# Kernel tuning notes

Hardware: AMD Instinct MI355X
Metric: run time of the kernel (lower is better)

The kernel has to match this reference:

```python
import jax, jax.numpy as jnp
import numpy as np

B, S, E = 4, 2048, 1024

def setup_inputs() -> dict:
    key = jax.random.key(0)
    ks = jax.random.split(key, 7)
    sc = 1.0 / np.sqrt(E)
    return {
        "x": jax.random.normal(ks[0], (B, S, E), dtype=jnp.float32),
        "wq_w": jax.random.normal(ks[1], (E, E), dtype=jnp.float32) * sc,
        "wq_b": jax.random.normal(ks[2], (E,), dtype=jnp.float32) * 0.01,
        "wk_w": jax.random.normal(ks[3], (E, E), dtype=jnp.float32) * sc,
        "wk_b": jax.random.normal(ks[4], (E,), dtype=jnp.float32) * 0.01,
        "wv_w": jax.random.normal(ks[5], (E, E), dtype=jnp.float32) * sc,
        "wv_b": jax.random.normal(ks[6], (E,), dtype=jnp.float32) * 0.01,
    }

def reference(x, wq_w, wq_b, wk_w, wk_b, wv_w, wv_b):
    # Linear projections (torch nn.Linear: y = x @ W^T + b)
    Q = jnp.einsum('bse,fe->bsf', x, wq_w) + wq_b
    K = jnp.einsum('bse,fe->bsf', x, wk_w) + wk_b
    V = jnp.einsum('bse,fe->bsf', x, wv_w) + wv_b
    # scaled dot-product attention, full [B, S, S] scores (single head)
    scores = jnp.einsum('bqe,bke->bqk', Q, K) / jnp.sqrt(jnp.asarray(Q.shape[-1], Q.dtype))
    attn = jax.nn.softmax(scores, axis=-1)
    return jnp.einsum('bqk,bke->bqe', attn, V)
```

## Files before the change

### kernel.cpp

```cpp
#include <hip/hip_runtime.h>
#include <hip/hip_bf16.h>
#include <stdint.h>

#define B_ 4
#define S_ 2048
#define E_ 1024


typedef __bf16 bf16;
typedef __attribute__((ext_vector_type(8))) __bf16 bf16x8;
typedef __attribute__((ext_vector_type(4))) float f32x4;
typedef __attribute__((ext_vector_type(4))) float float4v;
typedef __attribute__((ext_vector_type(4))) unsigned int uint4v;
typedef __attribute__((ext_vector_type(4))) unsigned short ushort4v;

__device__ inline unsigned short f2bf(float f) {
  union { float f; unsigned int u; } c; c.f = f;
  unsigned int u = c.u;
  unsigned int r = (u + 0x7FFFu + ((u >> 16) & 1u)) >> 16;
  return (unsigned short)r;
}

__device__ inline void load16_to_lds(const void* g, void* l) {
  __builtin_amdgcn_global_load_lds(
      (const __attribute__((address_space(1))) void*)g,
      (__attribute__((address_space(3))) void*)l,
      16, 0, 0);
}

__global__ __launch_bounds__(256) void cvt_all(
    const float* __restrict__ x, const float* __restrict__ w0,
    const float* __restrict__ w1, const float* __restrict__ w2,
    unsigned short* __restrict__ out, float* __restrict__ rowsum) {
  if (blockIdx.x >= 11264) {
    rowsum[(blockIdx.x - 11264) * 256 + threadIdx.x] = 0.f;
    return;
  }
  const long off = (long)blockIdx.x * 256 + threadIdx.x;
  const float* in;
  long ibase;
  if (blockIdx.x < 8192)       { in = x;  ibase = 0; }
  else if (blockIdx.x < 9216)  { in = w0; ibase = 8192L * 256; }
  else if (blockIdx.x < 10240) { in = w1; ibase = 9216L * 256; }
  else                         { in = w2; ibase = 10240L * 256; }
  float4v f = ((const float4v*)in)[off - ibase];
  ushort4v o;
  o.x = f2bf(f.x); o.y = f2bf(f.y); o.z = f2bf(f.z); o.w = f2bf(f.w);
  ((ushort4v*)out)[off] = o;
}

template <int MODE, int SWZ, int NXT>
__global__ __launch_bounds__(256, 4) void gemm_bt(
    const bf16* __restrict__ A, const bf16* __restrict__ B, void* __restrict__ Cv,
    const float* __restrict__ bias, const float* __restrict__ bias_b,
    const float* __restrict__ bias_v, unsigned short* __restrict__ VtOut,
    float* __restrict__ rowsum,
    int M, int N, int K, int lda, int ldb, int ldc,
    long sA, long sB, long sC, float scale, int nyt) {
  __shared__ bf16 As[128 * 64];
  __shared__ bf16 Bs[128 * 64];

  int xt, yt, zb;
  if (SWZ == 0) {
    xt = blockIdx.x; yt = blockIdx.y; zb = blockIdx.z;
  } else {
    const int flat = blockIdx.x;
    const int xcd = flat & 7;
    const int local = flat >> 3;
    zb = xcd >> 1;
    const int w = (xcd & 1) * (NXT * nyt / 2) + local;
    xt = w % NXT; yt = w / NXT;
  }

  A += (long)zb * sA;
  B += (long)zb * sB;
  const int tid = threadIdx.x;
  const int wave = tid >> 6;
  const int lane = tid & 63;
  const int lrow = lane & 15;
  const int quad = lane >> 4;
  const int row0 = yt * 128;
  const int col0 = xt * 128;
  const int wm = (wave >> 1) * 64;
  const int wn = (wave & 1) * 64;

  f32x4 acc[4][4] = {};

  const int r0 = wave * 8 + (lane >> 3);
  const int c0 = (lane & 7) * 8;

  const bf16* pA0 = A + (long)(row0 + r0) * lda + c0;
  const bf16* pA1 = pA0 + 32L * lda;
  const bf16* pA2 = pA0 + 64L * lda;
  const bf16* pA3 = pA0 + 96L * lda;
  const bf16* pB0 = B + (long)(col0 + r0) * ldb + c0;
  const bf16* pB1 = pB0 + 32L * ldb;
  const bf16* pB2 = pB0 + 64L * ldb;
  const bf16* pB3 = pB0 + 96L * ldb;
  bf16* ldsA = As + wave * 512;
  bf16* ldsB = Bs + wave * 512;

  for (int ks = 0; ks < K; ks += 64) {
    load16_to_lds(pA0, ldsA);
    load16_to_lds(pA1, ldsA + 2048);
    load16_to_lds(pA2, ldsA + 4096);
    load16_to_lds(pA3, ldsA + 6144);
    load16_to_lds(pB0, ldsB);
    load16_to_lds(pB1, ldsB + 2048);
    load16_to_lds(pB2, ldsB + 4096);
    load16_to_lds(pB3, ldsB + 6144);
    __syncthreads();
#pragma unroll
    for (int kk = 0; kk < 64; kk += 32) {
      bf16x8 af[4], bfr[4];
#pragma unroll
      for (int i = 0; i < 4; ++i)
        af[i] = *(const bf16x8*)(As + (wm + i * 16 + lrow) * 64 + kk + quad * 8);
#pragma unroll
      for (int j = 0; j < 4; ++j)
        bfr[j] = *(const bf16x8*)(Bs + (wn + j * 16 + lrow) * 64 + kk + quad * 8);
#pragma unroll
      for (int i = 0; i < 4; ++i)
#pragma unroll
        for (int j = 0; j < 4; ++j)
          acc[i][j] = __builtin_amdgcn_mfma_f32_16x16x32_bf16(af[i], bfr[j], acc[i][j], 0, 0, 0);
    }
    __syncthreads();
    pA0 += 64; pA1 += 64; pA2 += 64; pA3 += 64;
    pB0 += 64; pB1 += 64; pB2 += 64; pB3 += 64;
  }

  if (MODE == 8) {
    float* C = (float*)Cv + (long)zb * sC;
    const float* rs = rowsum + (long)zb * S_;
#pragma unroll
    for (int i = 0; i < 4; ++i) {
#pragma unroll
      for (int r = 0; r < 4; ++r) {
        const int row = row0 + wm + i * 16 + quad * 4 + r;
        const float inv = 1.0f / rs[row];
#pragma unroll
        for (int j = 0; j < 4; ++j) {
          const int col = col0 + wn + j * 16 + lrow;
          C[(long)row * ldc + col] = acc[i][j][r] * inv;
        }
      }
    }
  } else if (MODE == 7) {
    unsigned short* C = (unsigned short*)Cv + (long)zb * sC;
    float* rs = rowsum + (long)zb * S_;
    float rsump[4][4];
#pragma unroll
    for (int i = 0; i < 4; ++i)
#pragma unroll
      for (int r = 0; r < 4; ++r) rsump[i][r] = 0.f;
#pragma unroll
    for (int j = 0; j < 4; ++j) {
      const int col = col0 + wn + j * 16 + lrow;
#pragma unroll
      for (int i = 0; i < 4; ++i) {
#pragma unroll
        for (int r = 0; r < 4; ++r) {
          const int row = row0 + wm + i * 16 + quad * 4 + r;
          const float e = __expf(acc[i][j][r] * scale);
          rsump[i][r] += e;
          C[(long)row * ldc + col] = f2bf(e);
        }
      }
    }
#pragma unroll
    for (int i = 0; i < 4; ++i) {
#pragma unroll
      for (int r = 0; r < 4; ++r) {
        float v = rsump[i][r];
        v += __shfl_xor(v, 1);
        v += __shfl_xor(v, 2);
        v += __shfl_xor(v, 4);
        v += __shfl_xor(v, 8);
        if (lrow == 0)
          atomicAdd(&rs[row0 + wm + i * 16 + quad * 4 + r], v);
      }
    }
  } else {
    if (col0 < 2048) {
      unsigned short* C = (unsigned short*)Cv;
#pragma unroll
      for (int j = 0; j < 4; ++j) {
        const int col = col0 + wn + j * 16 + lrow;
        const float bcol = (col < E_) ? bias[col] : bias_b[col - E_];
#pragma unroll
        for (int i = 0; i < 4; ++i) {
#pragma unroll
          for (int r = 0; r < 4; ++r) {
            const int row = row0 + wm + i * 16 + quad * 4 + r;
            C[(long)row * ldc + col] = f2bf(acc[i][j][r] + bcol);
          }
        }
      }
    } else {
#pragma unroll
      for (int j = 0; j < 4; ++j) {
        const int e = col0 + wn + j * 16 + lrow - 2048;
        const float bv_ = bias_v[e];
#pragma unroll
        for (int i = 0; i < 4; ++i) {
          const int row = row0 + wm + i * 16 + quad * 4;
          ushort4v o;
          o.x = f2bf(acc[i][j][0] + bv_);
          o.y = f2bf(acc[i][j][1] + bv_);
          o.z = f2bf(acc[i][j][2] + bv_);
          o.w = f2bf(acc[i][j][3] + bv_);
          *(ushort4v*)(VtOut + (long)e * (B_ * S_) + row) = o;
        }
      }
    }
  }
}

extern "C" void kernel_launch(void* const* d_in, const int* in_sizes, int n_in,
                              void* d_out, int out_size, void* d_ws, size_t ws_size,
                              hipStream_t stream) {
  const float* x    = (const float*)d_in[0];
  const float* wq_w = (const float*)d_in[1];
  const float* wq_b = (const float*)d_in[2];
  const float* wk_w = (const float*)d_in[3];
  const float* wk_b = (const float*)d_in[4];
  const float* wv_w = (const float*)d_in[5];
  const float* wv_b = (const float*)d_in[6];
  float* out = (float*)d_out;

  const long NX = (long)B_ * S_ * E_;
  const long NW = (long)E_ * E_;
  char* ws = (char*)d_ws;
  bf16* xb  = (bf16*)ws; ws += NX * 2;
  bf16* wqb = (bf16*)ws; ws += NW * 2;
  bf16* wkb = (bf16*)ws; ws += NW * 2;
  bf16* wvb = (bf16*)ws; ws += NW * 2;
  bf16* QK  = (bf16*)ws; ws += 2 * NX * 2;
  bf16* Vt  = (bf16*)ws; ws += NX * 2;
  bf16* Sc  = (bf16*)ws; ws += (long)B_ * S_ * S_ * 2;
  float* rowsum = (float*)ws; ws += (long)B_ * S_ * 4;

  cvt_all<<<dim3(11272), 256, 0, stream>>>(
      x, wq_w, wk_w, wv_w, (unsigned short*)xb, rowsum);

  dim3 blk(256);
  gemm_bt<6, 0, 24><<<dim3((3 * E_) / 128, (B_ * S_) / 128, 1), blk, 0, stream>>>(
      xb, wqb, QK, wq_b, wk_b, wv_b, (unsigned short*)Vt, nullptr,
      B_ * S_, 3 * E_, E_, E_, E_, 2 * E_, 0, 0, 0, 1.f, 64);
  gemm_bt<7, 1, 16><<<dim3(1024, 1, 1), blk, 0, stream>>>(
      QK, QK + E_, Sc, nullptr, nullptr, nullptr, nullptr, rowsum,
      S_, S_, E_, 2 * E_, 2 * E_, S_,
      (long)S_ * 2 * E_, (long)S_ * 2 * E_, (long)S_ * S_, 0.03125f, 16);
  gemm_bt<8, 1, 8><<<dim3(512, 1, 1), blk, 0, stream>>>(
      Sc, Vt, out, nullptr, nullptr, nullptr, nullptr, rowsum,
      S_, E_, S_, S_, B_ * S_, E_,
      (long)S_ * S_, (long)S_, (long)S_ * E_, 1.f, 16);
}
```

Before: 256.5 us.

## Templatize GEMM N-tile width, use 64-wide tiles for PV, split Q/K buffers

```diff
diff --git a/kernel.cpp b/kernel.cpp
--- a/kernel.cpp
+++ b/kernel.cpp
@@ -49,7 +49,7 @@
   ((ushort4v*)out)[off] = o;
 }
 
-template <int MODE, int SWZ, int NXT>
+template <int MODE, int SWZ, int NXT, int BN>
 __global__ __launch_bounds__(256, 4) void gemm_bt(
     const bf16* __restrict__ A, const bf16* __restrict__ B, void* __restrict__ Cv,
     const float* __restrict__ bias, const float* __restrict__ bias_b,
@@ -57,8 +57,9 @@
     float* __restrict__ rowsum,
     int M, int N, int K, int lda, int ldb, int ldc,
     long sA, long sB, long sC, float scale, int nyt) {
+  constexpr int NJ = BN / 32;
   __shared__ bf16 As[128 * 64];
-  __shared__ bf16 Bs[128 * 64];
+  __shared__ bf16 Bs[BN * 64];
 
   int xt, yt, zb;
   if (SWZ == 0) {
@@ -80,11 +81,11 @@
   const int lrow = lane & 15;
   const int quad = lane >> 4;
   const int row0 = yt * 128;
-  const int col0 = xt * 128;
+  const int col0 = xt * BN;
   const int wm = (wave >> 1) * 64;
-  const int wn = (wave & 1) * 64;
-
-  f32x4 acc[4][4] = {};
+  const int wn = (wave & 1) * (BN / 2);
+
+  f32x4 acc[4][NJ] = {};
 
   const int r0 = wave * 8 + (lane >> 3);
   const int c0 = (lane & 7) * 8;
@@ -93,10 +94,10 @@
   const bf16* pA1 = pA0 + 32L * lda;
   const bf16* pA2 = pA0 + 64L * lda;
   const bf16* pA3 = pA0 + 96L * lda;
-  const bf16* pB0 = B + (long)(col0 + r0) * ldb + c0;
-  const bf16* pB1 = pB0 + 32L * ldb;
-  const bf16* pB2 = pB0 + 64L * ldb;
-  const bf16* pB3 = pB0 + 96L * ldb;
+  const bf16* pB[NJ];
+#pragma unroll
+  for (int h = 0; h < NJ; ++h)
+    pB[h] = B + (long)(col0 + r0 + 32 * h) * ldb + c0;
   bf16* ldsA = As + wave * 512;
   bf16* ldsB = Bs + wave * 512;
 
@@ -105,29 +106,29 @@
     load16_to_lds(pA1, ldsA + 2048);
     load16_to_lds(pA2, ldsA + 4096);
     load16_to_lds(pA3, ldsA + 6144);
-    load16_to_lds(pB0, ldsB);
-    load16_to_lds(pB1, ldsB + 2048);
-    load16_to_lds(pB2, ldsB + 4096);
-    load16_to_lds(pB3, ldsB + 6144);
+#pragma unroll
+    for (int h = 0; h < NJ; ++h)
+      load16_to_lds(pB[h], ldsB + h * 2048);
     __syncthreads();
 #pragma unroll
     for (int kk = 0; kk < 64; kk += 32) {
-      bf16x8 af[4], bfr[4];
+      bf16x8 af[4], bfr[NJ];
 #pragma unroll
       for (int i = 0; i < 4; ++i)
         af[i] = *(const bf16x8*)(As + (wm + i * 16 + lrow) * 64 + kk + quad * 8);
 #pragma unroll
-      for (int j = 0; j < 4; ++j)
+      for (int j = 0; j < NJ; ++j)
         bfr[j] = *(const bf16x8*)(Bs + (wn + j * 16 + lrow) * 64 + kk + quad * 8);
 #pragma unroll
       for (int i = 0; i < 4; ++i)
 #pragma unroll
-        for (int j = 0; j < 4; ++j)
+        for (int j = 0; j < NJ; ++j)
           acc[i][j] = __builtin_amdgcn_mfma_f32_16x16x32_bf16(af[i], bfr[j], acc[i][j], 0, 0, 0);
     }
     __syncthreads();
     pA0 += 64; pA1 += 64; pA2 += 64; pA3 += 64;
-    pB0 += 64; pB1 += 64; pB2 += 64; pB3 += 64;
+#pragma unroll
+    for (int h = 0; h < NJ; ++h) pB[h] += 64;
   }
 
   if (MODE == 8) {
@@ -140,7 +141,7 @@
         const int row = row0 + wm + i * 16 + quad * 4 + r;
         const float inv = 1.0f / rs[row];
 #pragma unroll
-        for (int j = 0; j < 4; ++j) {
+        for (int j = 0; j < NJ; ++j) {
           const int col = col0 + wn + j * 16 + lrow;
           C[(long)row * ldc + col] = acc[i][j][r] * inv;
         }
@@ -155,7 +156,7 @@
 #pragma unroll
       for (int r = 0; r < 4; ++r) rsump[i][r] = 0.f;
 #pragma unroll
-    for (int j = 0; j < 4; ++j) {
+    for (int j = 0; j < NJ; ++j) {
       const int col = col0 + wn + j * 16 + lrow;
 #pragma unroll
       for (int i = 0; i < 4; ++i) {
@@ -182,12 +183,18 @@
       }
     }
   } else {
-    if (col0 < 2048) {
-      unsigned short* C = (unsigned short*)Cv;
-#pragma unroll
-      for (int j = 0; j < 4; ++j) {
-        const int col = col0 + wn + j * 16 + lrow;
-        const float bcol = (col < E_) ? bias[col] : bias_b[col - E_];
+    if (col0 < 2 * E_) {
+      unsigned short* Cq = (unsigned short*)Cv;
+      unsigned short* Ck = Cq + (long)B_ * S_ * E_;
+      unsigned short* C;
+      const float* bb;
+      int cbase;
+      if (col0 < E_) { C = Cq; bb = bias;   cbase = col0; }
+      else           { C = Ck; bb = bias_b; cbase = col0 - E_; }
+#pragma unroll
+      for (int j = 0; j < NJ; ++j) {
+        const int col = cbase + wn + j * 16 + lrow;
+        const float bcol = bb[col];
 #pragma unroll
         for (int i = 0; i < 4; ++i) {
 #pragma unroll
@@ -199,8 +206,8 @@
       }
     } else {
 #pragma unroll
-      for (int j = 0; j < 4; ++j) {
-        const int e = col0 + wn + j * 16 + lrow - 2048;
+      for (int j = 0; j < NJ; ++j) {
+        const int e = col0 + wn + j * 16 + lrow - 2 * E_;
         const float bv_ = bias_v[e];
 #pragma unroll
         for (int i = 0; i < 4; ++i) {
@@ -236,7 +243,8 @@
   bf16* wqb = (bf16*)ws; ws += NW * 2;
   bf16* wkb = (bf16*)ws; ws += NW * 2;
   bf16* wvb = (bf16*)ws; ws += NW * 2;
-  bf16* QK  = (bf16*)ws; ws += 2 * NX * 2;
+  bf16* Qc  = (bf16*)ws; ws += NX * 2;
+  bf16* Kc  = (bf16*)ws; ws += NX * 2;
   bf16* Vt  = (bf16*)ws; ws += NX * 2;
   bf16* Sc  = (bf16*)ws; ws += (long)B_ * S_ * S_ * 2;
   float* rowsum = (float*)ws; ws += (long)B_ * S_ * 4;
@@ -245,14 +253,14 @@
       x, wq_w, wk_w, wv_w, (unsigned short*)xb, rowsum);
 
   dim3 blk(256);
-  gemm_bt<6, 0, 24><<<dim3((3 * E_) / 128, (B_ * S_) / 128, 1), blk, 0, stream>>>(
-      xb, wqb, QK, wq_b, wk_b, wv_b, (unsigned short*)Vt, nullptr,
-      B_ * S_, 3 * E_, E_, E_, E_, 2 * E_, 0, 0, 0, 1.f, 64);
-  gemm_bt<7, 1, 16><<<dim3(1024, 1, 1), blk, 0, stream>>>(
-      QK, QK + E_, Sc, nullptr, nullptr, nullptr, nullptr, rowsum,
-      S_, S_, E_, 2 * E_, 2 * E_, S_,
-      (long)S_ * 2 * E_, (long)S_ * 2 * E_, (long)S_ * S_, 0.03125f, 16);
-  gemm_bt<8, 1, 8><<<dim3(512, 1, 1), blk, 0, stream>>>(
+  gemm_bt<6, 0, 24, 128><<<dim3((3 * E_) / 128, (B_ * S_) / 128, 1), blk, 0, stream>>>(
+      xb, wqb, Qc, wq_b, wk_b, wv_b, (unsigned short*)Vt, nullptr,
+      B_ * S_, 3 * E_, E_, E_, E_, E_, 0, 0, 0, 1.f, 64);
+  gemm_bt<7, 1, 16, 128><<<dim3(1024, 1, 1), blk, 0, stream>>>(
+      Qc, Kc, Sc, nullptr, nullptr, nullptr, nullptr, rowsum,
+      S_, S_, E_, E_, E_, S_,
+      (long)S_ * E_, (long)S_ * E_, (long)S_ * S_, 0.03125f, 16);
+  gemm_bt<8, 1, 16, 64><<<dim3(1024, 1, 1), blk, 0, stream>>>(
       Sc, Vt, out, nullptr, nullptr, nullptr, nullptr, rowsum,
       S_, E_, S_, S_, B_ * S_, E_,
       (long)S_ * S_, (long)S_, (long)S_ * E_, 1.f, 16);
```

After: 262.1 us. 2.2% more time.
